# Kernel tuning notes

Measured on AMD Instinct MI355X. Metric: run time of the kernel, lower is better.

## Reference

```python
import jax, jax.numpy as jnp
import numpy as np
from jax import lax

NPOINT = 1024   # num_points (FPS centroids)
RADIUS = 0.2    # ball-query radius
K = 32          # samples per ball
FILTERS = [64, 64, 128]


def setup_inputs() -> dict:
    key = jax.random.key(0)
    ks = jax.random.split(key, 10)
    B, N, C = 16, 4096, 64
    xyz = jax.random.uniform(ks[0], (B, N, 3), dtype=jnp.float32)   # unit-cube cloud
    points = jax.random.normal(ks[1], (B, N, C), dtype=jnp.float32)
    inp = {"xyz": xyz, "points": points}
    cin = C + 3  # use_xyz=True concatenates relative xyz
    for i, f in enumerate(FILTERS):
        scale = np.sqrt(2.0 / (cin + f)).astype(np.float32)  # glorot_normal
        inp[f"w{i}"] = jax.random.normal(ks[2 + i], (cin, f), dtype=jnp.float32) * scale
        inp[f"b{i}"] = jnp.zeros((f,), dtype=jnp.float32)
        cin = f
    return inp


def farthest_point_sample(xyz, npoint):
    # Serial greedy FPS. xyz: [B,N,3] -> idx [B,npoint] int32
    B, N, _ = xyz.shape

    def body(carry, _):
        dist, far = carry                                   # [B,N], [B]
        centroid = jnp.take_along_axis(xyz, far[:, None, None], axis=1)  # [B,1,3]
        d = jnp.sum((xyz - centroid) ** 2, axis=-1)         # [B,N]
        dist = jnp.minimum(dist, d)
        nxt = jnp.argmax(dist, axis=-1).astype(jnp.int32)
        return (dist, nxt), far

    init = (jnp.full((B, N), 1e10, xyz.dtype), jnp.zeros((B,), jnp.int32))
    _, idxs = lax.scan(body, init, None, length=npoint)
    return idxs.T  # [B,npoint]


def query_ball(radius, nsample, xyz, new_xyz):
    # First-nsample-in-order points within radius; pad with first hit (CUDA semantics).
    B, N, _ = xyz.shape
    d2 = jnp.sum((new_xyz[:, :, None, :] - xyz[:, None, :, :]) ** 2, axis=-1)  # [B,S,N]
    mask = d2 <= radius * radius
    order = jnp.where(mask, jnp.arange(N, dtype=jnp.int32)[None, None, :], N)
    idx_sorted = jnp.sort(order, axis=-1)[..., :nsample]    # first K valid indices
    first = idx_sorted[..., :1]
    first = jnp.where(first < N, first, 0)                  # empty-ball fallback
    return jnp.where(idx_sorted < N, idx_sorted, first)     # [B,S,K]


def reference(xyz, points, w0, b0, w1, b1, w2, b2):
    B, N, _ = xyz.shape
    fps_idx = farthest_point_sample(xyz, NPOINT)                    # [B,S]
    new_xyz = jnp.take_along_axis(xyz, fps_idx[:, :, None], axis=1)  # [B,S,3]
    idx = query_ball(RADIUS, K, xyz, new_xyz)                        # [B,S,K]

    bix = jnp.arange(B)[:, None, None]
    grouped_xyz = xyz[bix, idx] - new_xyz[:, :, None, :]             # [B,S,K,3] recentered
    grouped_pts = points[bix, idx]                                   # [B,S,K,C]
    g = jnp.concatenate([grouped_pts, grouped_xyz], axis=-1)         # [B,S,K,C+3]

    for w, b in ((w0, b0), (w1, b1), (w2, b2)):                      # shared 1x1-conv MLP
        g = jax.nn.relu(jnp.einsum('bskc,cf->bskf', g, w) + b)
    new_points = jnp.max(g, axis=2)                                  # max-pool over ball
    return new_xyz, new_points
```

## Files before the change

kernel.cpp:

```cpp
#include <hip/hip_runtime.h>
#include <stdint.h>

#define BB 16
#define NN 4096
#define CC 64
#define NPOINT 1024
#define KK 32
#define F1 64
#define F2 64
#define F3 128

#define FPS_T 512
#define PPT (NN / FPS_T)

#if defined(__has_builtin)
#if __has_builtin(__builtin_amdgcn_update_dpp)
#define HAS_DPP 1
#endif
#endif

#ifdef HAS_DPP
template <int CTRL>
__device__ __forceinline__ unsigned long long dpp_move64(unsigned long long k) {
    int lo = __builtin_amdgcn_update_dpp(0, (int)(unsigned)k,         CTRL, 0xF, 0xF, false);
    int hi = __builtin_amdgcn_update_dpp(0, (int)(unsigned)(k >> 32), CTRL, 0xF, 0xF, false);
    return ((unsigned long long)(unsigned)hi << 32) | (unsigned)lo;
}
__device__ __forceinline__ unsigned long long wave_max_key(unsigned long long key) {
    unsigned long long o;
    o = dpp_move64<0x111>(key); if (o > key) key = o;
    o = dpp_move64<0x112>(key); if (o > key) key = o;
    o = dpp_move64<0x114>(key); if (o > key) key = o;
    o = dpp_move64<0x118>(key); if (o > key) key = o;
    o = dpp_move64<0x142>(key); if (o > key) key = o;
    o = dpp_move64<0x143>(key); if (o > key) key = o;
    return key;
}
#else
__device__ __forceinline__ unsigned long long wave_max_key(unsigned long long key) {
#pragma unroll
    for (int off = 32; off > 0; off >>= 1) {
        unsigned long long o = __shfl_xor(key, off, 64);
        if (o > key) key = o;
    }
    return key;
}
#endif

#define SMEM_BYTES 49664

__global__ __launch_bounds__(512)
void fused_kernel(const float* __restrict__ xyz,
                  const float* __restrict__ points,
                  const float* __restrict__ w0, const float* __restrict__ b0,
                  const float* __restrict__ w1, const float* __restrict__ b1,
                  const float* __restrict__ w2, const float* __restrict__ b2,
                  float* __restrict__ out_xyz,
                  float* __restrict__ out_points,
                  int* __restrict__ ctr) {
    __shared__ __align__(16) char smem[SMEM_BYTES];
    const int tid = threadIdx.x;

    if (blockIdx.x < BB) {
        asm volatile("s_setprio 3");
        float* xs = (float*)smem;
        float* ys = xs + NN;
        float* zs = ys + NN;
        unsigned long long (*wred)[FPS_T / 64] =
            (unsigned long long (*)[FPS_T / 64])(smem + 49152);
        float* cbuf = (float*)(smem + 49280);

        const int b = blockIdx.x;
        const int lane = tid & 63, wid = tid >> 6;
        const float* __restrict__ xb = xyz + (size_t)b * (NN * 3);

        float px[PPT], py[PPT], pz[PPT], dist[PPT];
#pragma unroll
        for (int t = 0; t < PPT; ++t) {
            int p = tid + t * FPS_T;
            px[t] = xb[p * 3 + 0];
            py[t] = xb[p * 3 + 1];
            pz[t] = xb[p * 3 + 2];
            xs[p] = px[t]; ys[p] = py[t]; zs[p] = pz[t];
            dist[t] = 1e10f;
        }
        __syncthreads();

        float cx = xs[0], cy = ys[0], cz = zs[0];
        float* xo = out_xyz + (size_t)b * NPOINT * 3;

        for (int i = 0; i < NPOINT; ++i) {
            if (tid == 0) {
                cbuf[(i & 7) * 3 + 0] = cx;
                cbuf[(i & 7) * 3 + 1] = cy;
                cbuf[(i & 7) * 3 + 2] = cz;
            }
            float bd = -1.0f; int bp = 0;
#pragma unroll
            for (int t = 0; t < PPT; ++t) {
                float dx = __fsub_rn(px[t], cx);
                float dy = __fsub_rn(py[t], cy);
                float dz = __fsub_rn(pz[t], cz);
                float d  = __fadd_rn(__fadd_rn(__fmul_rn(dx, dx), __fmul_rn(dy, dy)),
                                     __fmul_rn(dz, dz));
                float nd = fminf(dist[t], d);
                dist[t] = nd;
                if (nd > bd) { bd = nd; bp = tid + t * FPS_T; }
            }
            unsigned long long key = (((unsigned long long)__float_as_uint(bd)) << 32)
                                   | (unsigned int)(NN - 1 - bp);
            key = wave_max_key(key);
            if (lane == 63) wred[i & 1][wid] = key;
            __syncthreads();

            unsigned long long best = wred[i & 1][0];
#pragma unroll
            for (int w = 1; w < FPS_T / 64; ++w) {
                unsigned long long o = wred[i & 1][w];
                if (o > best) best = o;
            }
            int bi = (NN - 1) - (int)(best & 0xffffffffu);

            if (tid == 0 && (i & 7) == 7) {
                const float4* src = (const float4*)cbuf;
                float4* dst = (float4*)(xo + (size_t)(i - 7) * 3);
                dst[0] = src[0]; dst[1] = src[1]; dst[2] = src[2];
                dst[3] = src[3]; dst[4] = src[4]; dst[5] = src[5];
                __hip_atomic_store(&ctr[b * 16], i + 1,
                                   __ATOMIC_RELEASE, __HIP_MEMORY_SCOPE_AGENT);
            }
            cx = xs[bi]; cy = ys[bi]; cz = zs[bi];
        }
    } else {
        float (*gbuf)[68] = (float (*)[68])smem;
        float (*hbuf)[F1] = (float (*)[F1])(smem + 8704);
        float (*pmax)[F3] = (float (*)[F3])(smem + 16896);
        unsigned long long* cmask = (unsigned long long*)(smem + 20992);
        int* nbr = (int*)(smem + 21504);

        const int gi = blockIdx.x - BB;
        const int s = gi >> 4;
        const int b = gi & 15;
        const int g = b * NPOINT + s;
        const int f = tid & 63;
        const int wid = tid >> 6;

        if (tid == 0) {
            while (__hip_atomic_load(&ctr[b * 16], __ATOMIC_RELAXED,
                                     __HIP_MEMORY_SCOPE_AGENT) < s + 1)
                __builtin_amdgcn_s_sleep(2);
            (void)__hip_atomic_load(&ctr[b * 16], __ATOMIC_ACQUIRE,
                                    __HIP_MEMORY_SCOPE_AGENT);
        }
        __syncthreads();

        unsigned int ux = __hip_atomic_load((unsigned int*)&out_xyz[(size_t)g * 3 + 0],
                                            __ATOMIC_RELAXED, __HIP_MEMORY_SCOPE_AGENT);
        unsigned int uy = __hip_atomic_load((unsigned int*)&out_xyz[(size_t)g * 3 + 1],
                                            __ATOMIC_RELAXED, __HIP_MEMORY_SCOPE_AGENT);
        unsigned int uz = __hip_atomic_load((unsigned int*)&out_xyz[(size_t)g * 3 + 2],
                                            __ATOMIC_RELAXED, __HIP_MEMORY_SCOPE_AGENT);
        const float cx = __uint_as_float(ux);
        const float cy = __uint_as_float(uy);
        const float cz = __uint_as_float(uz);

        {
            const float* __restrict__ xb = xyz + (size_t)b * (NN * 3);
#pragma unroll
            for (int j = 0; j < 8; ++j) {
                int chunk = wid * 8 + j;
                int p = chunk * 64 + f;
                float x = xb[p * 3 + 0];
                float y = xb[p * 3 + 1];
                float z = xb[p * 3 + 2];
                float dx = __fsub_rn(cx, x);
                float dy = __fsub_rn(cy, y);
                float dz = __fsub_rn(cz, z);
                float d2 = __fadd_rn(__fadd_rn(__fmul_rn(dx, dx), __fmul_rn(dy, dy)),
                                     __fmul_rn(dz, dz));
                unsigned long long m = __ballot(d2 <= 0.04f);
                if (f == 0) cmask[chunk] = m;
            }
        }
        __syncthreads();

        if (tid < 64) {
            unsigned long long m = cmask[tid];
            int cnt = (int)__popcll(m);
            int v = cnt;
#pragma unroll
            for (int off = 1; off < 64; off <<= 1) {
                int u = __shfl_up(v, off, 64);
                if (tid >= off) v += u;
            }
            int excl = v - cnt;
            int total = __shfl(v, 63, 64);
            unsigned long long mm = m;
            int r = excl;
            while (mm && r < KK) {
                int bpos = __ffsll(mm) - 1;
                mm &= mm - 1;
                nbr[r++] = tid * 64 + bpos;
            }
            if (total < KK) {
                unsigned long long nz = __ballot(cnt > 0);
                int fchunk = __ffsll(nz) - 1;
                unsigned long long fm = cmask[fchunk];
                int first = fchunk * 64 + __ffsll(fm) - 1;
                if (tid >= total && tid < KK) nbr[tid] = first;
            }
        }
        __syncthreads();

        {
            const float* __restrict__ pb = points + (size_t)b * NN * CC;
#pragma unroll
            for (int m = 0; m < 4; ++m) {
                int k = wid + 8 * m;
                int idx = nbr[k] & (NN - 1);
                gbuf[k][f] = pb[(size_t)idx * CC + f];
            }
            if (tid < 96) {
                int k = tid & 31, q = tid >> 5;
                int idx = nbr[k] & (NN - 1);
                float v = xyz[((size_t)b * NN + idx) * 3 + q];
                float cq = (q == 0) ? cx : ((q == 1) ? cy : cz);
                gbuf[k][CC + q] = __fsub_rn(v, cq);
            }
        }
        __syncthreads();

        float acc[4];

#pragma unroll
        for (int m = 0; m < 4; ++m) acc[m] = 0.0f;
#pragma unroll 4
        for (int c4 = 0; c4 < 64; c4 += 4) {
            float wv0 = w0[(c4 + 0) * F1 + f];
            float wv1 = w0[(c4 + 1) * F1 + f];
            float wv2 = w0[(c4 + 2) * F1 + f];
            float wv3 = w0[(c4 + 3) * F1 + f];
#pragma unroll
            for (int m = 0; m < 4; ++m) {
                float4 gv = *(const float4*)&gbuf[wid + 8 * m][c4];
                acc[m] = fmaf(gv.x, wv0, acc[m]);
                acc[m] = fmaf(gv.y, wv1, acc[m]);
                acc[m] = fmaf(gv.z, wv2, acc[m]);
                acc[m] = fmaf(gv.w, wv3, acc[m]);
            }
        }
        {
            float wv0 = w0[64 * F1 + f];
            float wv1 = w0[65 * F1 + f];
            float wv2 = w0[66 * F1 + f];
#pragma unroll
            for (int m = 0; m < 4; ++m) {
                int k = wid + 8 * m;
                acc[m] = fmaf(gbuf[k][64], wv0, acc[m]);
                acc[m] = fmaf(gbuf[k][65], wv1, acc[m]);
                acc[m] = fmaf(gbuf[k][66], wv2, acc[m]);
            }
        }
        {
            float bb = b0[f];
#pragma unroll
            for (int m = 0; m < 4; ++m)
                hbuf[wid + 8 * m][f] = fmaxf(acc[m] + bb, 0.0f);
        }
        __syncthreads();

#pragma unroll
        for (int m = 0; m < 4; ++m) acc[m] = 0.0f;
#pragma unroll 4
        for (int c4 = 0; c4 < 64; c4 += 4) {
            float wv0 = w1[(c4 + 0) * F2 + f];
            float wv1 = w1[(c4 + 1) * F2 + f];
            float wv2 = w1[(c4 + 2) * F2 + f];
            float wv3 = w1[(c4 + 3) * F2 + f];
#pragma unroll
            for (int m = 0; m < 4; ++m) {
                float4 gv = *(const float4*)&hbuf[wid + 8 * m][c4];
                acc[m] = fmaf(gv.x, wv0, acc[m]);
                acc[m] = fmaf(gv.y, wv1, acc[m]);
                acc[m] = fmaf(gv.z, wv2, acc[m]);
                acc[m] = fmaf(gv.w, wv3, acc[m]);
            }
        }
        {
            float bb = b1[f];
#pragma unroll
            for (int m = 0; m < 4; ++m)
                gbuf[wid + 8 * m][f] = fmaxf(acc[m] + bb, 0.0f);
        }
        __syncthreads();

        float a0[4], a1[4];
#pragma unroll
        for (int m = 0; m < 4; ++m) { a0[m] = 0.0f; a1[m] = 0.0f; }
#pragma unroll 2
        for (int c4 = 0; c4 < 64; c4 += 4) {
            float w00 = w2[(c4 + 0) * F3 + f], w10 = w2[(c4 + 0) * F3 + f + 64];
            float w01 = w2[(c4 + 1) * F3 + f], w11 = w2[(c4 + 1) * F3 + f + 64];
            float w02 = w2[(c4 + 2) * F3 + f], w12 = w2[(c4 + 2) * F3 + f + 64];
            float w03 = w2[(c4 + 3) * F3 + f], w13 = w2[(c4 + 3) * F3 + f + 64];
#pragma unroll
            for (int m = 0; m < 4; ++m) {
                float4 gv = *(const float4*)&gbuf[wid + 8 * m][c4];
                a0[m] = fmaf(gv.x, w00, a0[m]);  a1[m] = fmaf(gv.x, w10, a1[m]);
                a0[m] = fmaf(gv.y, w01, a0[m]);  a1[m] = fmaf(gv.y, w11, a1[m]);
                a0[m] = fmaf(gv.z, w02, a0[m]);  a1[m] = fmaf(gv.z, w12, a1[m]);
                a0[m] = fmaf(gv.w, w03, a0[m]);  a1[m] = fmaf(gv.w, w13, a1[m]);
            }
        }
        {
            float pm0 = -1e30f, pm1 = -1e30f;
#pragma unroll
            for (int m = 0; m < 4; ++m) {
                pm0 = fmaxf(pm0, a0[m]);
                pm1 = fmaxf(pm1, a1[m]);
            }
            pmax[wid][f] = pm0;
            pmax[wid][f + 64] = pm1;
        }
        __syncthreads();
        if (tid < F3) {
            float v = pmax[0][tid];
#pragma unroll
            for (int w = 1; w < 8; ++w) v = fmaxf(v, pmax[w][tid]);
            v = fmaxf(v + b2[tid], 0.0f);
            out_points[(size_t)g * F3 + tid] = v;
        }
    }
}

extern "C" void kernel_launch(void* const* d_in, const int* in_sizes, int n_in,
                              void* d_out, int out_size, void* d_ws, size_t ws_size,
                              hipStream_t stream) {
    const float* xyz    = (const float*)d_in[0];
    const float* points = (const float*)d_in[1];
    const float* w0 = (const float*)d_in[2];
    const float* b0 = (const float*)d_in[3];
    const float* w1 = (const float*)d_in[4];
    const float* b1 = (const float*)d_in[5];
    const float* w2 = (const float*)d_in[6];
    const float* b2 = (const float*)d_in[7];

    float* out_xyz    = (float*)d_out;
    float* out_points = out_xyz + (size_t)BB * NPOINT * 3;
    int*   ctr        = (int*)d_ws;

    fused_kernel<<<BB + BB * NPOINT, 512, 0, stream>>>(
        xyz, points, w0, b0, w1, b1, w2, b2, out_xyz, out_points, ctr);
}
```

Before: 820.4 us.

## Pack FPS distance math into float2 ops and relax FPS-to-consumer signaling

The FPS loop now stores negated coordinates in two-wide float vectors, so the distance update can map to packed FP32 add and multiply instructions, with contraction disabled to keep rounding identical. The release-store and acquire-load handshake is replaced by relaxed atomic stores plus an explicit s_waitcnt. The counter is published one batch late, so the stores from the previous group of eight have drained before it advances. This is meant to shorten the serial FPS critical path and remove fence overhead. It relies on hand-placed waitcnt ordering for correctness and delays consumers by one batch. The shared-memory size also grows, which may lower occupancy for the consumer blocks.

```diff
diff --git a/kernel.cpp b/kernel.cpp
--- a/kernel.cpp
+++ b/kernel.cpp
@@ -12,6 +12,8 @@
 
 #define FPS_T 512
 #define PPT (NN / FPS_T)
+
+typedef float v2f __attribute__((ext_vector_type(2)));
 
 #if defined(__has_builtin)
 #if __has_builtin(__builtin_amdgcn_update_dpp)
@@ -47,7 +49,7 @@
 }
 #endif
 
-#define SMEM_BYTES 49664
+#define SMEM_BYTES 56320
 
 __global__ __launch_bounds__(512)
 void fused_kernel(const float* __restrict__ xyz,
@@ -74,15 +76,19 @@
         const int lane = tid & 63, wid = tid >> 6;
         const float* __restrict__ xb = xyz + (size_t)b * (NN * 3);
 
-        float px[PPT], py[PPT], pz[PPT], dist[PPT];
-#pragma unroll
-        for (int t = 0; t < PPT; ++t) {
-            int p = tid + t * FPS_T;
-            px[t] = xb[p * 3 + 0];
-            py[t] = xb[p * 3 + 1];
-            pz[t] = xb[p * 3 + 2];
-            xs[p] = px[t]; ys[p] = py[t]; zs[p] = pz[t];
-            dist[t] = 1e10f;
+        v2f nx[4], ny[4], nz[4], d2[4];
+#pragma unroll
+        for (int j = 0; j < 4; ++j) {
+            int p0 = tid + (2 * j) * FPS_T;
+            int p1 = tid + (2 * j + 1) * FPS_T;
+            float x0 = xb[p0 * 3 + 0], y0 = xb[p0 * 3 + 1], z0 = xb[p0 * 3 + 2];
+            float x1 = xb[p1 * 3 + 0], y1 = xb[p1 * 3 + 1], z1 = xb[p1 * 3 + 2];
+            xs[p0] = x0; ys[p0] = y0; zs[p0] = z0;
+            xs[p1] = x1; ys[p1] = y1; zs[p1] = z1;
+            nx[j].x = -x0; nx[j].y = -x1;
+            ny[j].x = -y0; ny[j].y = -y1;
+            nz[j].x = -z0; nz[j].y = -z1;
+            d2[j].x = 1e10f; d2[j].y = 1e10f;
         }
         __syncthreads();
 
@@ -96,16 +102,28 @@
                 cbuf[(i & 7) * 3 + 2] = cz;
             }
             float bd = -1.0f; int bp = 0;
-#pragma unroll
-            for (int t = 0; t < PPT; ++t) {
-                float dx = __fsub_rn(px[t], cx);
-                float dy = __fsub_rn(py[t], cy);
-                float dz = __fsub_rn(pz[t], cz);
-                float d  = __fadd_rn(__fadd_rn(__fmul_rn(dx, dx), __fmul_rn(dy, dy)),
-                                     __fmul_rn(dz, dz));
-                float nd = fminf(dist[t], d);
-                dist[t] = nd;
-                if (nd > bd) { bd = nd; bp = tid + t * FPS_T; }
+            {
+#pragma clang fp contract(off)
+                v2f cpx; cpx.x = cx; cpx.y = cx;
+                v2f cpy; cpy.x = cy; cpy.y = cy;
+                v2f cpz; cpz.x = cz; cpz.y = cz;
+#pragma unroll
+                for (int j = 0; j < 4; ++j) {
+                    v2f dx = cpx + nx[j];
+                    v2f dy = cpy + ny[j];
+                    v2f dz = cpz + nz[j];
+                    v2f xx = dx * dx;
+                    v2f yy = dy * dy;
+                    v2f zz = dz * dz;
+                    v2f ss = xx + yy;
+                    v2f dd = ss + zz;
+                    v2f nd;
+                    nd.x = fminf(d2[j].x, dd.x);
+                    nd.y = fminf(d2[j].y, dd.y);
+                    d2[j] = nd;
+                    if (nd.x > bd) { bd = nd.x; bp = tid + (2 * j) * FPS_T; }
+                    if (nd.y > bd) { bd = nd.y; bp = tid + (2 * j + 1) * FPS_T; }
+                }
             }
             unsigned long long key = (((unsigned long long)__float_as_uint(bd)) << 32)
                                    | (unsigned int)(NN - 1 - bp);
@@ -121,15 +139,25 @@
             }
             int bi = (NN - 1) - (int)(best & 0xffffffffu);
 
+            cx = xs[bi]; cy = ys[bi]; cz = zs[bi];
+
             if (tid == 0 && (i & 7) == 7) {
-                const float4* src = (const float4*)cbuf;
-                float4* dst = (float4*)(xo + (size_t)(i - 7) * 3);
-                dst[0] = src[0]; dst[1] = src[1]; dst[2] = src[2];
-                dst[3] = src[3]; dst[4] = src[4]; dst[5] = src[5];
-                __hip_atomic_store(&ctr[b * 16], i + 1,
-                                   __ATOMIC_RELEASE, __HIP_MEMORY_SCOPE_AGENT);
-            }
-            cx = xs[bi]; cy = ys[bi]; cz = zs[bi];
+                asm volatile("s_waitcnt vmcnt(0)" ::: "memory");
+                if (i > 7)
+                    __hip_atomic_store(&ctr[b * 16], i - 7,
+                                       __ATOMIC_RELAXED, __HIP_MEMORY_SCOPE_AGENT);
+                const unsigned* cbu = (const unsigned*)cbuf;
+                unsigned* dst = (unsigned*)(xo + (size_t)(i - 7) * 3);
+#pragma unroll
+                for (int q = 0; q < 24; ++q)
+                    __hip_atomic_store(dst + q, cbu[q],
+                                       __ATOMIC_RELAXED, __HIP_MEMORY_SCOPE_AGENT);
+            }
+        }
+        if (tid == 0) {
+            asm volatile("s_waitcnt vmcnt(0)" ::: "memory");
+            __hip_atomic_store(&ctr[b * 16], NPOINT,
+                               __ATOMIC_RELAXED, __HIP_MEMORY_SCOPE_AGENT);
         }
     } else {
         float (*gbuf)[68] = (float (*)[68])smem;
@@ -149,8 +177,6 @@
             while (__hip_atomic_load(&ctr[b * 16], __ATOMIC_RELAXED,
                                      __HIP_MEMORY_SCOPE_AGENT) < s + 1)
                 __builtin_amdgcn_s_sleep(2);
-            (void)__hip_atomic_load(&ctr[b * 16], __ATOMIC_ACQUIRE,
-                                    __HIP_MEMORY_SCOPE_AGENT);
         }
         __syncthreads();
 
```

New measurement: 857.9 us. 1.05x slower.
